# Kernel tuning notes

Measured on AMD Instinct MI355X. Metric: run time of the kernel, lower is better.

Reference implementation:

```python
import jax, jax.numpy as jnp
import numpy as np

B, K, T = 8, 88, 32768
NMS_KSIZE = 3
GAUSS_KSIZE = 7
GAUSS_STD = 1.0
VEL_PAD_L = 1
VEL_PAD_R = 1


def setup_inputs() -> dict:
    key = jax.random.key(0)
    k1, k2 = jax.random.split(key)
    onset_probs = jax.random.uniform(k1, (B, K, T), dtype=jnp.float32)
    velmap = jax.random.uniform(k2, (B, K, T), dtype=jnp.float32)
    pthresh = jnp.float32(0.5)
    return {"onset_probs": onset_probs, "velmap": velmap, "pthresh": pthresh}


def _gauss_blur1d(x, ksize, std):
    # depthwise gaussian blur along t, reflect padding, 'same' output
    center = (ksize - 1) / 2.0
    i = jnp.arange(ksize, dtype=jnp.float32)
    w = jnp.exp(-0.5 * ((i - center) / std) ** 2)
    w = w / w.sum()
    h = ksize // 2
    xp = jnp.pad(x, ((0, 0), (0, 0), (h, h)), mode="reflect")
    t = x.shape[-1]
    out = w[0] * jax.lax.dynamic_slice_in_dim(xp, 0, t, axis=2)
    for d in range(1, ksize):
        out = out + w[d] * jax.lax.dynamic_slice_in_dim(xp, d, t, axis=2)
    return out


def _nms1d(x, ksize, pthresh):
    # keep entries equal to the local max over a window of ksize (stride 1),
    # zero everything else, then threshold
    h = ksize // 2
    neg_inf = jnp.array(-jnp.inf, dtype=x.dtype)
    xp = jnp.pad(x, ((0, 0), (0, 0), (h, h)), constant_values=neg_inf)
    t = x.shape[-1]
    pooled = jax.lax.dynamic_slice_in_dim(xp, 0, t, axis=2)
    for d in range(1, ksize):
        pooled = jnp.maximum(pooled, jax.lax.dynamic_slice_in_dim(xp, d, t, axis=2))
    out = jnp.where(x == pooled, x, jnp.zeros((), x.dtype))
    out = jnp.where(out >= pthresh, out, jnp.zeros((), x.dtype))
    return out


def _windowed_vel(velmap, pad_l, pad_r):
    # mean of velmap over [t-pad_l, t+pad_r] with reflect padding (dense form
    # of read_velocities evaluated at every (b,k,t))
    total = pad_l + pad_r + 1
    vp = jnp.pad(velmap, ((0, 0), (0, 0), (pad_l, pad_r)), mode="reflect")
    t = velmap.shape[-1]
    acc = jax.lax.dynamic_slice_in_dim(vp, 0, t, axis=2)
    for d in range(1, total):
        acc = acc + jax.lax.dynamic_slice_in_dim(vp, d, t, axis=2)
    return acc / total


def reference(onset_probs, velmap, pthresh):
    prev_max = onset_probs.max()
    blurred = _gauss_blur1d(onset_probs, GAUSS_KSIZE, GAUSS_STD)
    probs = jnp.where(prev_max > 0, blurred, onset_probs)
    probs = _nms1d(probs, NMS_KSIZE, pthresh)
    vels = _windowed_vel(velmap, VEL_PAD_L, VEL_PAD_R)
    vels = jnp.where(probs > 0, vels, jnp.zeros((), vels.dtype))
    # dense equivalent of the nonzero()+gather+DataFrame: (prob, vel) at every
    # detected onset (nonzero entries of probs), zeros elsewhere
    return probs, vels
```

## Files before the change

kernel.cpp:

```cpp
#include <hip/hip_runtime.h>
#include <math.h>
#include <stdint.h>

#pragma clang fp contract(off)

#define T_DIM 32768
#define BLOCK 256

typedef float v4f __attribute__((ext_vector_type(4)));

#define FP_BARRIER(x) asm("" : "+v"(x))


__device__ __forceinline__ uint32_t float_key(float f) {
    uint32_t u = __float_as_uint(f);
    return (u & 0x80000000u) ? ~u : (u | 0x80000000u);
}

__device__ __forceinline__ int reflect_idx(int t) {
    if (t < 0) t = -t;
    if (t >= T_DIM) t = 2 * T_DIM - 2 - t;
    return t;
}

__device__ __forceinline__ float blur7(const float* __restrict__ w,
                                       const float* taps) {
    float acc = w[0] * taps[0];
    FP_BARRIER(acc);
    #pragma unroll
    for (int d = 1; d < 7; ++d) {
        float p = w[d] * taps[d];
        FP_BARRIER(p);
        acc = acc + p;
        FP_BARRIER(acc);
    }
    return acc;
}


__global__ void init_ws_kernel(uint32_t* ws) { ws[0] = 0u; }

__global__ __launch_bounds__(BLOCK) void max_kernel(const float* __restrict__ x,
                                                    uint32_t* __restrict__ ws, int n4) {
    int idx = blockIdx.x * blockDim.x + threadIdx.x;
    int stride = gridDim.x * blockDim.x;
    float m = -INFINITY;
    const v4f* x4 = reinterpret_cast<const v4f*>(x);
    for (int i = idx; i < n4; i += stride) {
        v4f v = x4[i];
        m = fmaxf(m, fmaxf(fmaxf(v.x, v.y), fmaxf(v.z, v.w)));
    }
    #pragma unroll
    for (int off = 32; off > 0; off >>= 1)
        m = fmaxf(m, __shfl_xor(m, off));
    __shared__ float red[BLOCK / 64];
    if ((threadIdx.x & 63) == 0) red[threadIdx.x >> 6] = m;
    __syncthreads();
    if (threadIdx.x == 0) {
        #pragma unroll
        for (int w = 1; w < BLOCK / 64; ++w) m = fmaxf(m, red[w]);
        atomicMax(ws, float_key(m));
    }
}

__global__ __launch_bounds__(BLOCK) void fused_kernel(
    const float* __restrict__ onset, const float* __restrict__ vel,
    const float* __restrict__ pth, const uint32_t* __restrict__ ws,
    float* __restrict__ probs_out, float* __restrict__ vels_out,
    float w0, float w1, float w2, float w3, float w4, float w5, float w6) {

    const int row = blockIdx.y;
    const int j0 = (blockIdx.x * BLOCK + threadIdx.x) * 4;
    const size_t base = (size_t)row * T_DIM;

    const bool sel = (ws[0] > 0x80000000u);
    const float pthresh = pth[0];
    const float w[7] = {w0, w1, w2, w3, w4, w5, w6};

    float pb[6], vv[6];

    if (j0 >= 4 && j0 + 8 <= T_DIM) {
        const v4f* x4 = reinterpret_cast<const v4f*>(onset + base + j0 - 4);
        v4f A = x4[0], Bv = x4[1], C = x4[2];
        float xx[12] = {A.x, A.y, A.z, A.w, Bv.x, Bv.y, Bv.z, Bv.w, C.x, C.y, C.z, C.w};

        const v4f* v4 = reinterpret_cast<const v4f*>(vel + base + j0 - 4);
        v4f Vm = v4[0], Vc = v4[1], Vp = v4[2];
        vv[0] = Vm.w; vv[1] = Vc.x; vv[2] = Vc.y; vv[3] = Vc.z; vv[4] = Vc.w; vv[5] = Vp.x;

        #pragma unroll
        for (int q = 0; q < 6; ++q) {
            float acc = blur7(w, &xx[q]);
            pb[q] = sel ? acc : xx[q + 3];
        }
    } else {
        const float* x = onset + base;
        const float* v = vel + base;
        #pragma unroll
        for (int q = 0; q < 6; ++q) {
            int t = j0 + q - 1;
            vv[q] = v[reflect_idx(t)];
            if (t < 0 || t >= T_DIM) {
                pb[q] = -INFINITY;
            } else {
                float taps[7];
                #pragma unroll
                for (int d = 0; d < 7; ++d)
                    taps[d] = x[reflect_idx(t - 3 + d)];
                float acc = blur7(w, taps);
                pb[q] = sel ? acc : x[t];
            }
        }
    }

    float po[4], vo[4];
    #pragma unroll
    for (int j = 0; j < 4; ++j) {
        float p = pb[j + 1];
        float pooled = fmaxf(fmaxf(pb[j], pb[j + 1]), pb[j + 2]);
        float o = (p == pooled) ? p : 0.0f;
        o = (o >= pthresh) ? o : 0.0f;
        po[j] = o;
        float a = (vv[j] + vv[j + 1]) + vv[j + 2];
        float vmean = a / 3.0f;
        vo[j] = (o > 0.0f) ? vmean : 0.0f;
    }

    v4f pov = {po[0], po[1], po[2], po[3]};
    v4f vov = {vo[0], vo[1], vo[2], vo[3]};
    __builtin_nontemporal_store(pov, reinterpret_cast<v4f*>(&probs_out[base + j0]));
    __builtin_nontemporal_store(vov, reinterpret_cast<v4f*>(&vels_out[base + j0]));
}


extern "C" void kernel_launch(void* const* d_in, const int* in_sizes, int n_in,
                              void* d_out, int out_size, void* d_ws, size_t ws_size,
                              hipStream_t stream) {
    const float* onset = (const float*)d_in[0];
    const float* vel   = (const float*)d_in[1];
    const float* pth   = (const float*)d_in[2];

    const int n = in_sizes[0];
    const int rows = n / T_DIM;
    float* probs_out = (float*)d_out;
    float* vels_out  = probs_out + (size_t)n;
    uint32_t* wsu = (uint32_t*)d_ws;

    float e[7];
    for (int i = 0; i < 7; ++i) {
        float xi = (float)i - 3.0f;
        float arg = -0.5f * (xi * xi);
        e[i] = (float)exp((double)arg);
    }
    float s = e[0];
    for (int i = 1; i < 7; ++i) s += e[i];
    float w[7];
    for (int i = 0; i < 7; ++i) w[i] = e[i] / s;

    init_ws_kernel<<<1, 1, 0, stream>>>(wsu);
    max_kernel<<<1024, BLOCK, 0, stream>>>(onset, wsu, n / 4);

    dim3 grid(T_DIM / (4 * BLOCK), rows);
    fused_kernel<<<grid, BLOCK, 0, stream>>>(
        onset, vel, pth, wsu, probs_out, vels_out,
        w[0], w[1], w[2], w[3], w[4], w[5], w[6]);
}
```

Measured before the change: 331.9 us.

## Fuse global max reduction into main kernel with speculative blur and fixup pass

Removes the separate max-reduction pass over onset_probs by computing per-block maxima inside the fused kernel and combining them with atomicMax. The main kernel now always applies the Gaussian blur on the assumption that the global max is positive. A fixup kernel recomputes the unblurred path when that assumption fails and exits early otherwise. This saves one full read of the input in exchange for an extra launch, an LDS reduction with a barrier, and atomics in every block.

```diff
diff --git a/kernel.cpp b/kernel.cpp
--- a/kernel.cpp
+++ b/kernel.cpp
@@ -40,32 +40,9 @@
 
 __global__ void init_ws_kernel(uint32_t* ws) { ws[0] = 0u; }
 
-__global__ __launch_bounds__(BLOCK) void max_kernel(const float* __restrict__ x,
-                                                    uint32_t* __restrict__ ws, int n4) {
-    int idx = blockIdx.x * blockDim.x + threadIdx.x;
-    int stride = gridDim.x * blockDim.x;
-    float m = -INFINITY;
-    const v4f* x4 = reinterpret_cast<const v4f*>(x);
-    for (int i = idx; i < n4; i += stride) {
-        v4f v = x4[i];
-        m = fmaxf(m, fmaxf(fmaxf(v.x, v.y), fmaxf(v.z, v.w)));
-    }
-    #pragma unroll
-    for (int off = 32; off > 0; off >>= 1)
-        m = fmaxf(m, __shfl_xor(m, off));
-    __shared__ float red[BLOCK / 64];
-    if ((threadIdx.x & 63) == 0) red[threadIdx.x >> 6] = m;
-    __syncthreads();
-    if (threadIdx.x == 0) {
-        #pragma unroll
-        for (int w = 1; w < BLOCK / 64; ++w) m = fmaxf(m, red[w]);
-        atomicMax(ws, float_key(m));
-    }
-}
-
 __global__ __launch_bounds__(BLOCK) void fused_kernel(
     const float* __restrict__ onset, const float* __restrict__ vel,
-    const float* __restrict__ pth, const uint32_t* __restrict__ ws,
+    const float* __restrict__ pth, uint32_t* __restrict__ ws,
     float* __restrict__ probs_out, float* __restrict__ vels_out,
     float w0, float w1, float w2, float w3, float w4, float w5, float w6) {
 
@@ -73,11 +50,11 @@
     const int j0 = (blockIdx.x * BLOCK + threadIdx.x) * 4;
     const size_t base = (size_t)row * T_DIM;
 
-    const bool sel = (ws[0] > 0x80000000u);
     const float pthresh = pth[0];
     const float w[7] = {w0, w1, w2, w3, w4, w5, w6};
 
     float pb[6], vv[6];
+    float lmax = -INFINITY;
 
     if (j0 >= 4 && j0 + 8 <= T_DIM) {
         const v4f* x4 = reinterpret_cast<const v4f*>(onset + base + j0 - 4);
@@ -88,14 +65,17 @@
         v4f Vm = v4[0], Vc = v4[1], Vp = v4[2];
         vv[0] = Vm.w; vv[1] = Vc.x; vv[2] = Vc.y; vv[3] = Vc.z; vv[4] = Vc.w; vv[5] = Vp.x;
 
-        #pragma unroll
-        for (int q = 0; q < 6; ++q) {
-            float acc = blur7(w, &xx[q]);
-            pb[q] = sel ? acc : xx[q + 3];
-        }
+        lmax = fmaxf(fmaxf(xx[4], xx[5]), fmaxf(xx[6], xx[7]));
+
+        #pragma unroll
+        for (int q = 0; q < 6; ++q)
+            pb[q] = blur7(w, &xx[q]);
     } else {
         const float* x = onset + base;
         const float* v = vel + base;
+        #pragma unroll
+        for (int j = 0; j < 4; ++j)
+            lmax = fmaxf(lmax, x[j0 + j]);
         #pragma unroll
         for (int q = 0; q < 6; ++q) {
             int t = j0 + q - 1;
@@ -107,8 +87,7 @@
                 #pragma unroll
                 for (int d = 0; d < 7; ++d)
                     taps[d] = x[reflect_idx(t - 3 + d)];
-                float acc = blur7(w, taps);
-                pb[q] = sel ? acc : x[t];
+                pb[q] = blur7(w, taps);
             }
         }
     }
@@ -130,6 +109,59 @@
     v4f vov = {vo[0], vo[1], vo[2], vo[3]};
     __builtin_nontemporal_store(pov, reinterpret_cast<v4f*>(&probs_out[base + j0]));
     __builtin_nontemporal_store(vov, reinterpret_cast<v4f*>(&vels_out[base + j0]));
+
+    #pragma unroll
+    for (int off = 32; off > 0; off >>= 1)
+        lmax = fmaxf(lmax, __shfl_xor(lmax, off));
+    __shared__ float red[BLOCK / 64];
+    if ((threadIdx.x & 63) == 0) red[threadIdx.x >> 6] = lmax;
+    __syncthreads();
+    if (threadIdx.x == 0) {
+        #pragma unroll
+        for (int i = 1; i < BLOCK / 64; ++i) lmax = fmaxf(lmax, red[i]);
+        atomicMax(ws, float_key(lmax));
+    }
+}
+
+__global__ __launch_bounds__(BLOCK) void fixup_kernel(
+    const float* __restrict__ onset, const float* __restrict__ vel,
+    const float* __restrict__ pth, const uint32_t* __restrict__ ws,
+    float* __restrict__ probs_out, float* __restrict__ vels_out) {
+
+    if (ws[0] > 0x80000000u) return;
+
+    const int row = blockIdx.y;
+    const int j0 = (blockIdx.x * BLOCK + threadIdx.x) * 4;
+    const size_t base = (size_t)row * T_DIM;
+    const float pthresh = pth[0];
+    const float* x = onset + base;
+    const float* v = vel + base;
+
+    float pb[6], vv[6];
+    #pragma unroll
+    for (int q = 0; q < 6; ++q) {
+        int t = j0 + q - 1;
+        vv[q] = v[reflect_idx(t)];
+        pb[q] = (t < 0 || t >= T_DIM) ? -INFINITY : x[t];
+    }
+
+    float po[4], vo[4];
+    #pragma unroll
+    for (int j = 0; j < 4; ++j) {
+        float p = pb[j + 1];
+        float pooled = fmaxf(fmaxf(pb[j], pb[j + 1]), pb[j + 2]);
+        float o = (p == pooled) ? p : 0.0f;
+        o = (o >= pthresh) ? o : 0.0f;
+        po[j] = o;
+        float a = (vv[j] + vv[j + 1]) + vv[j + 2];
+        float vmean = a / 3.0f;
+        vo[j] = (o > 0.0f) ? vmean : 0.0f;
+    }
+
+    v4f pov = {po[0], po[1], po[2], po[3]};
+    v4f vov = {vo[0], vo[1], vo[2], vo[3]};
+    *reinterpret_cast<v4f*>(&probs_out[base + j0]) = pov;
+    *reinterpret_cast<v4f*>(&vels_out[base + j0]) = vov;
 }
 
 
@@ -157,11 +189,12 @@
     float w[7];
     for (int i = 0; i < 7; ++i) w[i] = e[i] / s;
 
+    dim3 grid(T_DIM / (4 * BLOCK), rows);
+
     init_ws_kernel<<<1, 1, 0, stream>>>(wsu);
-    max_kernel<<<1024, BLOCK, 0, stream>>>(onset, wsu, n / 4);
-
-    dim3 grid(T_DIM / (4 * BLOCK), rows);
     fused_kernel<<<grid, BLOCK, 0, stream>>>(
         onset, vel, pth, wsu, probs_out, vels_out,
         w[0], w[1], w[2], w[3], w[4], w[5], w[6]);
-}
+    fixup_kernel<<<grid, BLOCK, 0, stream>>>(
+        onset, vel, pth, wsu, probs_out, vels_out);
+}
```

Result: slower. 483.3 us (+45.6%).
